# Optimization experiments

Hardware: AMD Instinct MI355X
Metric: run time of the kernel (lower is better)

## Reference

```python
import jax, jax.numpy as jnp
import numpy as np

N_MOLS = 32768        # number of molecules in the batch
N_ATOMS = 4_194_304   # total atoms across all molecules (~128 atoms/mol)


def setup_inputs() -> dict:
    key = jax.random.key(0)
    k1, k2, k3 = jax.random.split(key, 3)
    xyz = jax.random.normal(k1, (N_ATOMS, 3), dtype=jnp.float32)
    # sorted segment ids == torch.split by per-molecule counts
    segment_ids = jnp.sort(jax.random.randint(k2, (N_ATOMS,), 0, N_MOLS))
    # minimal differentiable per-atom energy head (stand-in for upstream net)
    w = jax.random.normal(k3, (3,), dtype=jnp.float32)
    return {"xyz": xyz, "segment_ids": segment_ids, "w": w}


def reference(xyz, segment_ids, w):
    # atomwise energy: [N_ATOMS]; segment-sum -> per-molecule energy [N_MOLS]
    def energy_fn(x):
        atomwise = jnp.tanh(x @ w)
        return jax.ops.segment_sum(atomwise, segment_ids, num_segments=N_MOLS)

    energy, vjp_fn = jax.vjp(energy_fn, xyz)
    # compute_grad(output=energy, inputs=xyz) with ones grad_outputs
    (energy_grad,) = vjp_fn(jnp.ones_like(energy))
    return energy, energy_grad
```

## Files before the change

kernel.cpp:

```cpp
#include <hip/hip_runtime.h>

#define N_MOLS   32768
#define NATOMS   4194304
#define BLOCK    256
#define APT      4
#define APB      (BLOCK * APT)

typedef float  f32x4 __attribute__((ext_vector_type(4)));
typedef int    i32x4 __attribute__((ext_vector_type(4)));

__device__ __forceinline__ float fast_tanh(float x) {
    float e = __expf(2.0f * x);
    return 1.0f - 2.0f * __builtin_amdgcn_rcpf(e + 1.0f);
}

__global__ __launch_bounds__(BLOCK)
void SumPool_5325759447404_kernel(const float* __restrict__ xyz,
                                  const int*   __restrict__ seg,
                                  const float* __restrict__ w,
                                  float* __restrict__ energy,
                                  float* __restrict__ grad) {
    const int a0   = (blockIdx.x * BLOCK + threadIdx.x) * APT;
    const int lane = threadIdx.x & 63;

    const float w0 = w[0], w1 = w[1], w2 = w[2];

    const f32x4* __restrict__ xyz4 = (const f32x4*)(xyz + (size_t)a0 * 3);
    const f32x4 p = xyz4[0];
    const f32x4 q = xyz4[1];
    const f32x4 r = xyz4[2];

    const float t0 = fast_tanh(p.x * w0 + p.y * w1 + p.z * w2);
    const float t1 = fast_tanh(p.w * w0 + q.x * w1 + q.y * w2);
    const float t2 = fast_tanh(q.z * w0 + q.w * w1 + r.x * w2);
    const float t3 = fast_tanh(r.y * w0 + r.z * w1 + r.w * w2);

    const float d0 = 1.0f - t0 * t0;
    const float d1 = 1.0f - t1 * t1;
    const float d2 = 1.0f - t2 * t2;
    const float d3 = 1.0f - t3 * t3;

    f32x4 g0, g1, g2;
    g0.x = d0 * w0; g0.y = d0 * w1; g0.z = d0 * w2; g0.w = d1 * w0;
    g1.x = d1 * w1; g1.y = d1 * w2; g1.z = d2 * w0; g1.w = d2 * w1;
    g2.x = d2 * w2; g2.y = d3 * w0; g2.z = d3 * w1; g2.w = d3 * w2;

    f32x4* __restrict__ grad4 = (f32x4*)(grad + (size_t)a0 * 3);
    grad4[0] = g0;
    grad4[1] = g1;
    grad4[2] = g2;

    const i32x4 ids = *(const i32x4*)(seg + a0);

    float acc = t0;
    int   cur = ids.x;
    if (ids.y == cur) { acc += t1; } else { atomicAdd(&energy[cur], acc); cur = ids.y; acc = t1; }
    if (ids.z == cur) { acc += t2; } else { atomicAdd(&energy[cur], acc); cur = ids.z; acc = t2; }
    if (ids.w == cur) { acc += t3; } else { atomicAdd(&energy[cur], acc); cur = ids.w; acc = t3; }

    float v  = acc;
    int   id = cur;
    #pragma unroll
    for (int off = 1; off < 64; off <<= 1) {
        float vv = __shfl_up(v, off, 64);
        int   ii = __shfl_up(id, off, 64);
        if (lane >= off && ii == id) v += vv;
    }
    const int nid   = __shfl_down(id, 1, 64);
    const bool last = (lane == 63) || (nid != id);
    if (last) atomicAdd(&energy[id], v);
}

extern "C" void kernel_launch(void* const* d_in, const int* in_sizes, int n_in,
                              void* d_out, int out_size, void* d_ws, size_t ws_size,
                              hipStream_t stream) {
    const float* xyz = (const float*)d_in[0];
    const int*   seg = (const int*)d_in[1];
    const float* w   = (const float*)d_in[2];

    float* energy = (float*)d_out;
    float* grad   = energy + N_MOLS;


    const int nblocks = NATOMS / APB;
    SumPool_5325759447404_kernel<<<nblocks, BLOCK, 0, stream>>>(xyz, seg, w, energy, grad);
}
```

Measured before the change: 113.7 us.

## Stage xyz loads and grad stores through padded LDS for coalesced global access

Instead of each thread loading three strided float4 vectors directly (stride 48 bytes), the block loads its tile contiguously with float4 per thread, stages it in padded LDS, and reads back per-thread atoms. The gradient takes the same path in reverse: it is written to LDS, then stored contiguously to global memory. The goal is fully coalesced global transactions. The cost is two block barriers and added LDS traffic, which may lower occupancy.

New measurement: 109.9 us. -3.3%, faster.

```diff
diff --git a/kernel.cpp b/kernel.cpp
--- a/kernel.cpp
+++ b/kernel.cpp
@@ -5,6 +5,8 @@
 #define BLOCK    256
 #define APT      4
 #define APB      (BLOCK * APT)
+#define TILE_F4  (APB * 3 / 4)
+#define LDS_BYTES (12288 + 2048)
 
 typedef float  f32x4 __attribute__((ext_vector_type(4)));
 typedef int    i32x4 __attribute__((ext_vector_type(4)));
@@ -14,21 +16,39 @@
     return 1.0f - 2.0f * __builtin_amdgcn_rcpf(e + 1.0f);
 }
 
+__device__ __forceinline__ int pad_off(int j) {
+    return 16 * j + (j / 6) * 16;
+}
+
 __global__ __launch_bounds__(BLOCK)
 void SumPool_5325759447404_kernel(const float* __restrict__ xyz,
                                   const int*   __restrict__ seg,
                                   const float* __restrict__ w,
                                   float* __restrict__ energy,
                                   float* __restrict__ grad) {
-    const int a0   = (blockIdx.x * BLOCK + threadIdx.x) * APT;
-    const int lane = threadIdx.x & 63;
+    __shared__ __align__(16) unsigned char lds[LDS_BYTES];
+
+    const int t    = threadIdx.x;
+    const int lane = t & 63;
+    const int a0   = (blockIdx.x * BLOCK + t) * APT;
 
     const float w0 = w[0], w1 = w[1], w2 = w[2];
 
-    const f32x4* __restrict__ xyz4 = (const f32x4*)(xyz + (size_t)a0 * 3);
-    const f32x4 p = xyz4[0];
-    const f32x4 q = xyz4[1];
-    const f32x4 r = xyz4[2];
+    const f32x4* __restrict__ src = (const f32x4*)xyz + (size_t)blockIdx.x * TILE_F4;
+    const f32x4 v0 = src[t];
+    const f32x4 v1 = src[t + 256];
+    const f32x4 v2 = src[t + 512];
+
+    *(f32x4*)(lds + pad_off(t))       = v0;
+    *(f32x4*)(lds + pad_off(t + 256)) = v1;
+    *(f32x4*)(lds + pad_off(t + 512)) = v2;
+
+    __syncthreads();
+
+    const int r0 = 48 * t + (t >> 1) * 16;
+    const f32x4 p = *(const f32x4*)(lds + r0);
+    const f32x4 q = *(const f32x4*)(lds + r0 + 16);
+    const f32x4 r = *(const f32x4*)(lds + r0 + 32);
 
     const float t0 = fast_tanh(p.x * w0 + p.y * w1 + p.z * w2);
     const float t1 = fast_tanh(p.w * w0 + q.x * w1 + q.y * w2);
@@ -45,10 +65,9 @@
     g1.x = d1 * w1; g1.y = d1 * w2; g1.z = d2 * w0; g1.w = d2 * w1;
     g2.x = d2 * w2; g2.y = d3 * w0; g2.z = d3 * w1; g2.w = d3 * w2;
 
-    f32x4* __restrict__ grad4 = (f32x4*)(grad + (size_t)a0 * 3);
-    grad4[0] = g0;
-    grad4[1] = g1;
-    grad4[2] = g2;
+    *(f32x4*)(lds + r0)      = g0;
+    *(f32x4*)(lds + r0 + 16) = g1;
+    *(f32x4*)(lds + r0 + 32) = g2;
 
     const i32x4 ids = *(const i32x4*)(seg + a0);
 
@@ -69,6 +88,13 @@
     const int nid   = __shfl_down(id, 1, 64);
     const bool last = (lane == 63) || (nid != id);
     if (last) atomicAdd(&energy[id], v);
+
+    __syncthreads();
+
+    f32x4* __restrict__ dst = (f32x4*)grad + (size_t)blockIdx.x * TILE_F4;
+    dst[t]       = *(const f32x4*)(lds + pad_off(t));
+    dst[t + 256] = *(const f32x4*)(lds + pad_off(t + 256));
+    dst[t + 512] = *(const f32x4*)(lds + pad_off(t + 512));
 }
 
 extern "C" void kernel_launch(void* const* d_in, const int* in_sizes, int n_in,
```

## Stage xyz/grad through padded LDS for coalesced loads and stores, multi-tile blocks

Applied to the files above, without the earlier changes.

Each block now handles four tiles of 1024 atoms. The xyz data is loaded with fully coalesced float4 accesses (consecutive threads read consecutive float4s), transposed through a padded, double-buffered LDS tile, and the gradient is written back through the same LDS for coalesced stores. The next tile's loads are prefetched into registers while the current tile is processed. The aim is better global memory coalescing and more latency hiding, at the cost of LDS traffic, two barriers per tile and four times fewer blocks.

Result: faster. 108.7 us (median of 2 runs) (-4.4%).

```diff
diff --git a/kernel.cpp b/kernel.cpp
--- a/kernel.cpp
+++ b/kernel.cpp
@@ -5,6 +5,10 @@
 #define BLOCK    256
 #define APT      4
 #define APB      (BLOCK * APT)
+#define TILE_F4  (APB * 3 / 4)
+#define TPB      4
+#define NBLOCKS  (NATOMS / (APB * TPB))
+#define LDS_TILE (12288 + 2048)
 
 typedef float  f32x4 __attribute__((ext_vector_type(4)));
 typedef int    i32x4 __attribute__((ext_vector_type(4)));
@@ -14,61 +18,105 @@
     return 1.0f - 2.0f * __builtin_amdgcn_rcpf(e + 1.0f);
 }
 
+__device__ __forceinline__ int pad_off(int j) {
+    return 16 * j + (j / 6) * 16;
+}
+
 __global__ __launch_bounds__(BLOCK)
 void SumPool_5325759447404_kernel(const float* __restrict__ xyz,
                                   const int*   __restrict__ seg,
                                   const float* __restrict__ w,
                                   float* __restrict__ energy,
                                   float* __restrict__ grad) {
-    const int a0   = (blockIdx.x * BLOCK + threadIdx.x) * APT;
-    const int lane = threadIdx.x & 63;
+    __shared__ __align__(16) unsigned char lds[2][LDS_TILE];
+
+    const int t    = threadIdx.x;
+    const int lane = t & 63;
 
     const float w0 = w[0], w1 = w[1], w2 = w[2];
 
-    const f32x4* __restrict__ xyz4 = (const f32x4*)(xyz + (size_t)a0 * 3);
-    const f32x4 p = xyz4[0];
-    const f32x4 q = xyz4[1];
-    const f32x4 r = xyz4[2];
+    const f32x4* __restrict__ src = (const f32x4*)xyz;
+    f32x4*       __restrict__ dst = (f32x4*)grad;
 
-    const float t0 = fast_tanh(p.x * w0 + p.y * w1 + p.z * w2);
-    const float t1 = fast_tanh(p.w * w0 + q.x * w1 + q.y * w2);
-    const float t2 = fast_tanh(q.z * w0 + q.w * w1 + r.x * w2);
-    const float t3 = fast_tanh(r.y * w0 + r.z * w1 + r.w * w2);
+    const int tile0 = blockIdx.x * TPB;
 
-    const float d0 = 1.0f - t0 * t0;
-    const float d1 = 1.0f - t1 * t1;
-    const float d2 = 1.0f - t2 * t2;
-    const float d3 = 1.0f - t3 * t3;
+    size_t base = (size_t)tile0 * TILE_F4;
+    f32x4 n0 = src[base + t];
+    f32x4 n1 = src[base + t + 256];
+    f32x4 n2 = src[base + t + 512];
+    i32x4 nid = *(const i32x4*)(seg + (size_t)tile0 * APB + APT * t);
 
-    f32x4 g0, g1, g2;
-    g0.x = d0 * w0; g0.y = d0 * w1; g0.z = d0 * w2; g0.w = d1 * w0;
-    g1.x = d1 * w1; g1.y = d1 * w2; g1.z = d2 * w0; g1.w = d2 * w1;
-    g2.x = d2 * w2; g2.y = d3 * w0; g2.z = d3 * w1; g2.w = d3 * w2;
+    #pragma unroll
+    for (int tt = 0; tt < TPB; ++tt) {
+        const int tile = tile0 + tt;
+        const f32x4 v0 = n0, v1 = n1, v2 = n2;
+        const i32x4 ids = nid;
 
-    f32x4* __restrict__ grad4 = (f32x4*)(grad + (size_t)a0 * 3);
-    grad4[0] = g0;
-    grad4[1] = g1;
-    grad4[2] = g2;
+        if (tt + 1 < TPB) {
+            const size_t nb = (size_t)(tile + 1) * TILE_F4;
+            n0  = src[nb + t];
+            n1  = src[nb + t + 256];
+            n2  = src[nb + t + 512];
+            nid = *(const i32x4*)(seg + (size_t)(tile + 1) * APB + APT * t);
+        }
 
-    const i32x4 ids = *(const i32x4*)(seg + a0);
+        unsigned char* __restrict__ B = lds[tt & 1];
 
-    float acc = t0;
-    int   cur = ids.x;
-    if (ids.y == cur) { acc += t1; } else { atomicAdd(&energy[cur], acc); cur = ids.y; acc = t1; }
-    if (ids.z == cur) { acc += t2; } else { atomicAdd(&energy[cur], acc); cur = ids.z; acc = t2; }
-    if (ids.w == cur) { acc += t3; } else { atomicAdd(&energy[cur], acc); cur = ids.w; acc = t3; }
+        *(f32x4*)(B + pad_off(t))       = v0;
+        *(f32x4*)(B + pad_off(t + 256)) = v1;
+        *(f32x4*)(B + pad_off(t + 512)) = v2;
 
-    float v  = acc;
-    int   id = cur;
-    #pragma unroll
-    for (int off = 1; off < 64; off <<= 1) {
-        float vv = __shfl_up(v, off, 64);
-        int   ii = __shfl_up(id, off, 64);
-        if (lane >= off && ii == id) v += vv;
+        __syncthreads();
+
+        const int r0 = 48 * t + (t >> 1) * 16;
+        const f32x4 p = *(const f32x4*)(B + r0);
+        const f32x4 q = *(const f32x4*)(B + r0 + 16);
+        const f32x4 r = *(const f32x4*)(B + r0 + 32);
+
+        const float t0 = fast_tanh(p.x * w0 + p.y * w1 + p.z * w2);
+        const float t1 = fast_tanh(p.w * w0 + q.x * w1 + q.y * w2);
+        const float t2 = fast_tanh(q.z * w0 + q.w * w1 + r.x * w2);
+        const float t3 = fast_tanh(r.y * w0 + r.z * w1 + r.w * w2);
+
+        const float d0 = 1.0f - t0 * t0;
+        const float d1 = 1.0f - t1 * t1;
+        const float d2 = 1.0f - t2 * t2;
+        const float d3 = 1.0f - t3 * t3;
+
+        f32x4 g0, g1, g2;
+        g0.x = d0 * w0; g0.y = d0 * w1; g0.z = d0 * w2; g0.w = d1 * w0;
+        g1.x = d1 * w1; g1.y = d1 * w2; g1.z = d2 * w0; g1.w = d2 * w1;
+        g2.x = d2 * w2; g2.y = d3 * w0; g2.z = d3 * w1; g2.w = d3 * w2;
+
+        *(f32x4*)(B + r0)      = g0;
+        *(f32x4*)(B + r0 + 16) = g1;
+        *(f32x4*)(B + r0 + 32) = g2;
+
+        float acc = t0;
+        int   cur = ids.x;
+        if (ids.y == cur) { acc += t1; } else { atomicAdd(&energy[cur], acc); cur = ids.y; acc = t1; }
+        if (ids.z == cur) { acc += t2; } else { atomicAdd(&energy[cur], acc); cur = ids.z; acc = t2; }
+        if (ids.w == cur) { acc += t3; } else { atomicAdd(&energy[cur], acc); cur = ids.w; acc = t3; }
+
+        float v  = acc;
+        int   id = cur;
+        #pragma unroll
+        for (int off = 1; off < 64; off <<= 1) {
+            float vv = __shfl_up(v, off, 64);
+            int   ii = __shfl_up(id, off, 64);
+            if (lane >= off && ii == id) v += vv;
+        }
+        const int nid2  = __shfl_down(id, 1, 64);
+        const bool last = (lane == 63) || (nid2 != id);
+        if (last) atomicAdd(&energy[id], v);
+
+        __syncthreads();
+
+        const size_t ob = (size_t)tile * TILE_F4;
+        dst[ob + t]       = *(const f32x4*)(B + pad_off(t));
+        dst[ob + t + 256] = *(const f32x4*)(B + pad_off(t + 256));
+        dst[ob + t + 512] = *(const f32x4*)(B + pad_off(t + 512));
     }
-    const int nid   = __shfl_down(id, 1, 64);
-    const bool last = (lane == 63) || (nid != id);
-    if (last) atomicAdd(&energy[id], v);
 }
 
 extern "C" void kernel_launch(void* const* d_in, const int* in_sizes, int n_in,
@@ -82,6 +130,5 @@
     float* grad   = energy + N_MOLS;
 
 
-    const int nblocks = NATOMS / APB;
-    SumPool_5325759447404_kernel<<<nblocks, BLOCK, 0, stream>>>(xyz, seg, w, energy, grad);
+    SumPool_5325759447404_kernel<<<NBLOCKS, BLOCK, 0, stream>>>(xyz, seg, w, energy, grad);
 }
```
